# Optimization experiments

Hardware: AMD Instinct MI355X
Metric: run time of the kernel (lower is better)

The kernel has to match this reference:

```python
import jax, jax.numpy as jnp
import numpy as np

N = 50000        # nodes
E = 800000       # edges (avg degree 16)
MUL = 32         # multiplicity of 0e and 1o node-feature irreps
NA = 16          # node attr scalars (species embedding)
NB = 8           # edge radial basis size
FC_H = 64        # radial MLP hidden width
NPATH = 5        # tp paths: 0e*0e->0e, 0e*1o->1o, 1o*0e->1o, 1o*1o->0e, 1o*1o->1o
AVG_NEI = 16.0


def setup_inputs() -> dict:
    k = jax.random.split(jax.random.key(0), 16)
    return dict(
        node_feats=jax.random.normal(k[0], (N, 4 * MUL), jnp.float32),   # 32x0e + 32x1o
        node_attrs=jax.random.normal(k[1], (N, NA), jnp.float32),
        edge_embedding=jax.random.uniform(k[2], (E, NB), jnp.float32),
        edge_attrs=jax.random.normal(k[3], (E, 4), jnp.float32),         # SH l=0 (1) + l=1 (3)
        edge_src=jax.random.randint(k[4], (E,), 0, N),
        edge_dst=jax.random.randint(k[5], (E,), 0, N),
        W1_s=jax.random.normal(k[6], (MUL, MUL), jnp.float32) / np.sqrt(MUL),
        W1_v=jax.random.normal(k[7], (MUL, MUL), jnp.float32) / np.sqrt(MUL),
        fc_w1=jax.random.normal(k[8], (NB, FC_H), jnp.float32) / np.sqrt(NB),
        fc_b1=jnp.zeros((FC_H,), jnp.float32),
        fc_w2=jax.random.normal(k[9], (FC_H, NPATH * MUL), jnp.float32) / np.sqrt(FC_H),
        W2_s=jax.random.normal(k[10], (2 * MUL, 2 * MUL), jnp.float32) / np.sqrt(2 * MUL),
        W2_v=jax.random.normal(k[11], (3 * MUL, MUL), jnp.float32) / np.sqrt(3 * MUL),
        Wsc_s=jax.random.normal(k[12], (MUL, NA, 2 * MUL), jnp.float32) / np.sqrt(MUL * NA),
        Wsc_v=jax.random.normal(k[13], (MUL, NA, MUL), jnp.float32) / np.sqrt(MUL * NA),
    )


def reference(node_feats, node_attrs, edge_embedding, edge_attrs,
              edge_src, edge_dst, W1_s, W1_v, fc_w1, fc_b1, fc_w2,
              W2_s, W2_v, Wsc_s, Wsc_v):
    n = node_feats.shape[0]
    s = node_feats[:, :MUL]                        # [N, mul]     0e scalars
    v = node_feats[:, MUL:].reshape(n, MUL, 3)     # [N, mul, 3]  1o vectors

    # linear_1: per-irrep multiplicity mixing
    x_s = s @ W1_s
    x_v = jnp.einsum('nuc,uv->nvc', v, W1_v)

    # radial network -> per-edge tensor-product path weights (uvu, mul_in2 = 1)
    w = jax.nn.silu(edge_embedding @ fc_w1 + fc_b1) @ fc_w2   # [E, 5*mul]
    w00, w01, w10, w11s, w11v = [w[:, i * MUL:(i + 1) * MUL] for i in range(NPATH)]

    sh0 = edge_attrs[:, :1]     # [E, 1]  l=0
    sh1 = edge_attrs[:, 1:4]    # [E, 3]  l=1

    xs = x_s[edge_src]          # [E, mul]      gather source-node features
    xv = x_v[edge_src]          # [E, mul, 3]

    # Clebsch-Gordan tensor-product messages
    m_s0 = w00 * xs * sh0                                              # 0e x 0e -> 0e
    m_s1 = w11s * jnp.einsum('euc,ec->eu', xv, sh1) / np.sqrt(3.0)     # 1o x 1o -> 0e
    m_v0 = (w01 * xs)[:, :, None] * sh1[:, None, :]                    # 0e x 1o -> 1o
    m_v1 = w10[:, :, None] * xv * sh0[:, :, None]                      # 1o x 0e -> 1o
    m_v2 = w11v[:, :, None] * jnp.cross(
        xv, jnp.broadcast_to(sh1[:, None, :], xv.shape)) / np.sqrt(2.0)  # 1o x 1o -> 1o

    # scatter-sum to destination nodes, normalized by sqrt(avg num neighbors)
    inv = 1.0 / np.sqrt(AVG_NEI)
    a_s = jax.ops.segment_sum(jnp.concatenate([m_s0, m_s1], axis=1),
                              edge_dst, num_segments=n) * inv           # [N, 2*mul]
    a_v = jax.ops.segment_sum(jnp.concatenate([m_v0, m_v1, m_v2], axis=1),
                              edge_dst, num_segments=n) * inv           # [N, 3*mul, 3]

    # linear_2: mix tp paths into gated irreps (2*mul scalars + mul vectors)
    y_s = a_s @ W2_s
    y_v = jnp.einsum('nuc,uo->noc', a_v, W2_v)

    # self-connection: fully-connected tp of input feats with scalar node attrs
    y_s = y_s + jnp.einsum('nu,na,uao->no', s, node_attrs, Wsc_s)
    y_v = y_v + jnp.einsum('nuc,na,uao->noc', v, node_attrs, Wsc_v)

    # gate: first mul scalars -> silu output; next mul scalars -> silu gates on vectors
    out_s = jax.nn.silu(y_s[:, :MUL])
    gates = jax.nn.silu(y_s[:, MUL:])
    out_v = y_v * gates[:, :, None]

    out = jnp.concatenate([out_s, out_v.reshape(n, 3 * MUL)], axis=1)
    return node_feats + out   # resnet (irreps match)
```

## Files before the change

### kernel.cpp

```cpp
#include <hip/hip_runtime.h>

#define NN 50000
#define NE 800000

__device__ __forceinline__ float silu_f(float x) { return x / (1.0f + __expf(-x)); }

__global__ __launch_bounds__(256) void k_node_transform(
    const float* __restrict__ node_feats,
    const float* __restrict__ W1_s,
    const float* __restrict__ W1_v,
    float* __restrict__ xf)
{
    __shared__ float sW1s[32 * 32];
    __shared__ float sW1v[32 * 32];
    __shared__ float sfeat[8][128];
    int t = threadIdx.x;
    for (int i = t; i < 1024; i += 256) { sW1s[i] = W1_s[i]; sW1v[i] = W1_v[i]; }
    int nodeBase = blockIdx.x * 8;
    for (int i = t; i < 8 * 128; i += 256) {
        int nn = nodeBase + (i >> 7);
        sfeat[i >> 7][i & 127] = (nn < NN) ? node_feats[(long)nn * 128 + (i & 127)] : 0.0f;
    }
    __syncthreads();
    int g = t >> 5, o = t & 31;
    int n = nodeBase + g;
    if (n >= NN) return;
    float accs = 0.f, acc0 = 0.f, acc1 = 0.f, acc2 = 0.f;
#pragma unroll
    for (int u = 0; u < 32; ++u) {
        float su  = sfeat[g][u];
        float vu0 = sfeat[g][32 + u * 3 + 0];
        float vu1 = sfeat[g][32 + u * 3 + 1];
        float vu2 = sfeat[g][32 + u * 3 + 2];
        float ws = sW1s[u * 32 + o];
        float wv = sW1v[u * 32 + o];
        accs += su * ws;
        acc0 += vu0 * wv;
        acc1 += vu1 * wv;
        acc2 += vu2 * wv;
    }
    float4 r; r.x = accs; r.y = acc0; r.z = acc1; r.w = acc2;
    *(float4*)&xf[((long)n * 32 + o) * 4] = r;
}

__global__ __launch_bounds__(256) void k_hist(const int* __restrict__ edge_dst,
                                              int* __restrict__ counts)
{
    int e = blockIdx.x * 256 + threadIdx.x;
    if (e < NE) atomicAdd(&counts[edge_dst[e]], 1);
}

__global__ __launch_bounds__(1024) void k_scan(const int* __restrict__ counts,
                                               int* __restrict__ row_ptr,
                                               int* __restrict__ cursor)
{
    __shared__ int wsum[16];
    __shared__ int carry_s;
    int t = threadIdx.x;
    int lane = t & 63, w = t >> 6;
    if (t == 0) carry_s = 0;
    __syncthreads();
    for (int base = 0; base < NN; base += 1024) {
        int i = base + t;
        int v = (i < NN) ? counts[i] : 0;
        int s = v;
#pragma unroll
        for (int d = 1; d < 64; d <<= 1) {
            int o = __shfl_up(s, d, 64);
            if (lane >= d) s += o;
        }
        if (lane == 63) wsum[w] = s;
        __syncthreads();
        if (w == 0) {
            int ws = (lane < 16) ? wsum[lane] : 0;
#pragma unroll
            for (int d = 1; d < 16; d <<= 1) {
                int o = __shfl_up(ws, d, 64);
                if (lane >= d) ws += o;
            }
            if (lane < 16) wsum[lane] = ws;
        }
        __syncthreads();
        int excl = (s - v) + ((w > 0) ? wsum[w - 1] : 0) + carry_s;
        if (i < NN) { row_ptr[i] = excl; cursor[i] = excl; }
        int total = wsum[15];
        __syncthreads();
        if (t == 0) carry_s += total;
        __syncthreads();
    }
    if (t == 0) row_ptr[NN] = carry_s;
}

__global__ __launch_bounds__(256) void k_fill(const int* __restrict__ edge_dst,
                                              int* __restrict__ cursor,
                                              int* __restrict__ edge_ids)
{
    int e = blockIdx.x * 256 + threadIdx.x;
    if (e < NE) {
        int slot = atomicAdd(&cursor[edge_dst[e]], 1);
        edge_ids[slot] = e;
    }
}

__global__ __launch_bounds__(256, 3) void k_gather_t(
    const float* __restrict__ edge_embedding,
    const float* __restrict__ edge_attrs,
    const int*   __restrict__ edge_src,
    const float* __restrict__ fc_w1,
    const float* __restrict__ fc_b1,
    const float* __restrict__ fc_w2,
    const float* __restrict__ xf,
    const int*   __restrict__ row_ptr,
    const int*   __restrict__ edge_ids,
    const float* __restrict__ node_feats,
    const float* __restrict__ node_attrs,
    const float* __restrict__ W2_s,
    const float* __restrict__ W2_v,
    const float* __restrict__ Wsc_s,
    const float* __restrict__ Wsc_v,
    float* __restrict__ out)
{
    __shared__ __align__(16) float sw2t[160 * 68];
    __shared__ __align__(16) float hbuf[8][256];

    int t = threadIdx.x;
    for (int i = t; i < 64 * 160; i += 256) {
        int j = i / 160, c = i - j * 160;
        sw2t[c * 68 + j] = fc_w2[i];
    }
    __syncthreads();

    int g = t >> 5, lane = t & 31;
    int n = blockIdx.x * 8 + g;

    float w1a[8], w1b[8];
#pragma unroll
    for (int q = 0; q < 8; ++q) {
        w1a[q] = fc_w1[q * 64 + lane];
        w1b[q] = fc_w1[q * 64 + 32 + lane];
    }
    float b1a = fc_b1[lane], b1b = fc_b1[32 + lane];

    int start = row_ptr[n];
    int end   = row_ptr[n + 1];

    float as0 = 0.f, as1 = 0.f;
    float av[9];
#pragma unroll
    for (int p = 0; p < 9; ++p) av[p] = 0.f;

    float* hb = &hbuf[g][0];
    const float4* xf4 = (const float4*)xf;
    const float INV_SQRT3 = 0.5773502691896258f;
    const float INV_SQRT2 = 0.7071067811865476f;
    const float INV_NEI   = 0.25f;

    for (int i = start; i < end; i += 4) {
        int ne = end - i;
        int eid[4];
#pragma unroll
        for (int k = 0; k < 4; ++k) eid[k] = edge_ids[(k < ne) ? (i + k) : i];

        int srcv[4];
#pragma unroll
        for (int k = 0; k < 4; ++k) srcv[k] = edge_src[eid[k]];
        float4 at[4];
#pragma unroll
        for (int k = 0; k < 4; ++k) at[k] = *(const float4*)&edge_attrs[(long)eid[k] * 4];
        float4 xv[4];
#pragma unroll
        for (int k = 0; k < 4; ++k) xv[k] = xf4[(long)srcv[k] * 32 + lane];
        float em[4][8];
#pragma unroll
        for (int k = 0; k < 4; ++k) {
            *(float4*)&em[k][0] = *(const float4*)&edge_embedding[(long)eid[k] * 8];
            *(float4*)&em[k][4] = *(const float4*)&edge_embedding[(long)eid[k] * 8 + 4];
        }

#pragma unroll
        for (int k = 0; k < 4; ++k) {
            float h0 = b1a, h1 = b1b;
#pragma unroll
            for (int q = 0; q < 8; ++q) {
                float e = em[k][q];
                h0 += e * w1a[q];
                h1 += e * w1b[q];
            }
            hb[k * 64 + lane]      = silu_f(h0);
            hb[k * 64 + 32 + lane] = silu_f(h1);
        }

        float acc[5][4];
#pragma unroll
        for (int p = 0; p < 5; ++p)
#pragma unroll
            for (int k = 0; k < 4; ++k) acc[p][k] = 0.f;

#pragma unroll 2
        for (int jb = 0; jb < 16; ++jb) {
            float4 w0 = *(const float4*)&sw2t[(0 * 32 + lane) * 68 + jb * 4];
            float4 w1 = *(const float4*)&sw2t[(1 * 32 + lane) * 68 + jb * 4];
            float4 w2 = *(const float4*)&sw2t[(2 * 32 + lane) * 68 + jb * 4];
            float4 w3 = *(const float4*)&sw2t[(3 * 32 + lane) * 68 + jb * 4];
            float4 w4 = *(const float4*)&sw2t[(4 * 32 + lane) * 68 + jb * 4];
#pragma unroll
            for (int k = 0; k < 4; ++k) {
                float4 h4 = *(const float4*)&hb[k * 64 + jb * 4];
                acc[0][k] += h4.x * w0.x + h4.y * w0.y + h4.z * w0.z + h4.w * w0.w;
                acc[1][k] += h4.x * w1.x + h4.y * w1.y + h4.z * w1.z + h4.w * w1.w;
                acc[2][k] += h4.x * w2.x + h4.y * w2.y + h4.z * w2.z + h4.w * w2.w;
                acc[3][k] += h4.x * w3.x + h4.y * w3.y + h4.z * w3.z + h4.w * w3.w;
                acc[4][k] += h4.x * w4.x + h4.y * w4.y + h4.z * w4.z + h4.w * w4.w;
            }
        }

#pragma unroll
        for (int k = 0; k < 4; ++k) {
            if (k >= ne) break;
            float4 a4 = at[k];
            float xs  = xv[k].x;
            float xv0 = xv[k].y, xv1 = xv[k].z, xv2 = xv[k].w;
            float w00 = acc[0][k], w01 = acc[1][k], w10 = acc[2][k];
            float w11s = acc[3][k], w11v = acc[4][k];

            as0 += w00 * xs * a4.x;
            float dot = xv0 * a4.y + xv1 * a4.z + xv2 * a4.w;
            as1 += w11s * dot * INV_SQRT3;
            float t01 = w01 * xs;
            av[0] += t01 * a4.y; av[1] += t01 * a4.z; av[2] += t01 * a4.w;
            float t10 = w10 * a4.x;
            av[3] += t10 * xv0; av[4] += t10 * xv1; av[5] += t10 * xv2;
            float k2 = w11v * INV_SQRT2;
            av[6] += k2 * (xv1 * a4.w - xv2 * a4.z);
            av[7] += k2 * (xv2 * a4.y - xv0 * a4.w);
            av[8] += k2 * (xv0 * a4.z - xv1 * a4.y);
        }
    }

    __syncthreads();
    float* epi = sw2t + (g << 9);

    epi[lane]      = as0 * INV_NEI;
    epi[32 + lane] = as1 * INV_NEI;
#pragma unroll
    for (int p = 0; p < 3; ++p)
#pragma unroll
        for (int c = 0; c < 3; ++c)
            epi[64 + (p * 32 + lane) * 3 + c] = av[p * 3 + c] * INV_NEI;

    *(float4*)&hb[lane * 4] = *(const float4*)&node_feats[(long)n * 128 + lane * 4];
    if (lane < 16) hb[128 + lane] = node_attrs[(long)n * 16 + lane];

    int o = lane;
    float ys0 = 0.f, ys1 = 0.f, yv0 = 0.f, yv1 = 0.f, yv2 = 0.f;

#pragma unroll 8
    for (int u = 0; u < 64; ++u) {
        float as = epi[u];
        ys0 += as * W2_s[u * 64 + o];
        ys1 += as * W2_s[u * 64 + 32 + o];
    }
#pragma unroll 8
    for (int u = 0; u < 96; ++u) {
        float wv = W2_v[u * 32 + o];
        yv0 += epi[64 + u * 3 + 0] * wv;
        yv1 += epi[64 + u * 3 + 1] * wv;
        yv2 += epi[64 + u * 3 + 2] * wv;
    }

    float att[16];
#pragma unroll
    for (int a = 0; a < 16; ++a) att[a] = hb[128 + a];

    for (int u = 0; u < 32; ++u) {
        const float* Wsp = &Wsc_s[u * 1024 + o];
        const float* Wvp = &Wsc_v[u * 512 + o];
        float t0 = 0.f, t1 = 0.f, tv = 0.f;
#pragma unroll
        for (int a = 0; a < 16; ++a) {
            float aa = att[a];
            t0 += aa * Wsp[a * 64];
            t1 += aa * Wsp[a * 64 + 32];
            tv += aa * Wvp[a * 32];
        }
        float su = hb[u];
        ys0 += su * t0;
        ys1 += su * t1;
        float vv0 = hb[32 + u * 3 + 0];
        float vv1 = hb[32 + u * 3 + 1];
        float vv2 = hb[32 + u * 3 + 2];
        yv0 += vv0 * tv;
        yv1 += vv1 * tv;
        yv2 += vv2 * tv;
    }

    float os   = silu_f(ys0);
    float gate = silu_f(ys1);
    long base = (long)n * 128;
    out[base + o] = hb[o] + os;
    out[base + 32 + o * 3 + 0] = hb[32 + o * 3 + 0] + yv0 * gate;
    out[base + 32 + o * 3 + 1] = hb[32 + o * 3 + 1] + yv1 * gate;
    out[base + 32 + o * 3 + 2] = hb[32 + o * 3 + 2] + yv2 * gate;
}

extern "C" void kernel_launch(void* const* d_in, const int* in_sizes, int n_in,
                              void* d_out, int out_size, void* d_ws, size_t ws_size,
                              hipStream_t stream) {
    const float* node_feats     = (const float*)d_in[0];
    const float* node_attrs     = (const float*)d_in[1];
    const float* edge_embedding = (const float*)d_in[2];
    const float* edge_attrs     = (const float*)d_in[3];
    const int*   edge_src       = (const int*)d_in[4];
    const int*   edge_dst       = (const int*)d_in[5];
    const float* W1_s  = (const float*)d_in[6];
    const float* W1_v  = (const float*)d_in[7];
    const float* fc_w1 = (const float*)d_in[8];
    const float* fc_b1 = (const float*)d_in[9];
    const float* fc_w2 = (const float*)d_in[10];
    const float* W2_s  = (const float*)d_in[11];
    const float* W2_v  = (const float*)d_in[12];
    const float* Wsc_s = (const float*)d_in[13];
    const float* Wsc_v = (const float*)d_in[14];
    float* out = (float*)d_out;

    float* ws  = (float*)d_ws;
    float* xf  = ws;
    int* ibase    = (int*)(ws + (long)NN * 128);
    int* counts   = ibase;
    int* row_ptr  = ibase + NN;
    int* cursor   = ibase + 2 * NN + 1;
    int* edge_ids = ibase + 3 * NN + 1;

    hipMemsetAsync(counts, 0, (size_t)NN * sizeof(int), stream);
    k_hist<<<(NE + 255) / 256, 256, 0, stream>>>(edge_dst, counts);
    k_node_transform<<<(NN + 7) / 8, 256, 0, stream>>>(node_feats, W1_s, W1_v, xf);
    k_scan<<<1, 1024, 0, stream>>>(counts, row_ptr, cursor);
    k_fill<<<(NE + 255) / 256, 256, 0, stream>>>(edge_dst, cursor, edge_ids);
    k_gather_t<<<NN / 8, 256, 0, stream>>>(edge_embedding, edge_attrs, edge_src,
                                           fc_w1, fc_b1, fc_w2, xf,
                                           row_ptr, edge_ids,
                                           node_feats, node_attrs,
                                           W2_s, W2_v, Wsc_s, Wsc_v, out);
}
```

Measured before the change: 921.6 us.

## Use fp16 packed dot products for radial MLP second layer with 8-edge batches

The radial MLP hidden activations and the fc_w2 matrix are stored in shared memory as fp16 and combined with v_dot2 (fdot2) instructions that accumulate in fp32. This halves LDS traffic and instruction count for the dominant per-edge 64x160 matmul. Edges are now processed 8 at a time, the hidden-unit layout is interleaved in pairs, and the shared pool is shrunk and reused for the epilogue so occupancy can rise to 4 blocks per CU. The cost is reduced precision in the path weights and higher register pressure from the larger accumulator array.

```diff
diff --git a/kernel.cpp b/kernel.cpp
--- a/kernel.cpp
+++ b/kernel.cpp
@@ -3,7 +3,18 @@
 #define NN 50000
 #define NE 800000
 
+typedef _Float16 half2t __attribute__((ext_vector_type(2)));
+union H16 { float4 f; half2t p[4]; };
+
 __device__ __forceinline__ float silu_f(float x) { return x / (1.0f + __expf(-x)); }
+
+__device__ __forceinline__ float fdot2(half2t a, half2t b, float c) {
+#if __has_builtin(__builtin_amdgcn_fdot2)
+    return __builtin_amdgcn_fdot2(a, b, c, false);
+#else
+    return c + (float)a.x * (float)b.x + (float)a.y * (float)b.y;
+#endif
+}
 
 __global__ __launch_bounds__(256) void k_node_transform(
     const float* __restrict__ node_feats,
@@ -102,7 +113,10 @@
     }
 }
 
-__global__ __launch_bounds__(256, 3) void k_gather_t(
+#define SW2_HBYTES (160 * 72 * 2)
+#define POOL_BYTES (SW2_HBYTES + 8 * 8 * 128)
+
+__global__ __launch_bounds__(256, 4) void k_gather_t(
     const float* __restrict__ edge_embedding,
     const float* __restrict__ edge_attrs,
     const int*   __restrict__ edge_src,
@@ -120,13 +134,14 @@
     const float* __restrict__ Wsc_v,
     float* __restrict__ out)
 {
-    __shared__ __align__(16) float sw2t[160 * 68];
-    __shared__ __align__(16) float hbuf[8][256];
+    __shared__ __align__(16) unsigned char pool[POOL_BYTES];
+    _Float16* swp = (_Float16*)pool;
+    half2t*   hhp = (half2t*)(pool + SW2_HBYTES);
 
     int t = threadIdx.x;
     for (int i = t; i < 64 * 160; i += 256) {
         int j = i / 160, c = i - j * 160;
-        sw2t[c * 68 + j] = fc_w2[i];
+        swp[c * 72 + j] = (_Float16)fc_w2[i];
     }
     __syncthreads();
 
@@ -136,10 +151,10 @@
     float w1a[8], w1b[8];
 #pragma unroll
     for (int q = 0; q < 8; ++q) {
-        w1a[q] = fc_w1[q * 64 + lane];
-        w1b[q] = fc_w1[q * 64 + 32 + lane];
-    }
-    float b1a = fc_b1[lane], b1b = fc_b1[32 + lane];
+        w1a[q] = fc_w1[q * 64 + 2 * lane];
+        w1b[q] = fc_w1[q * 64 + 2 * lane + 1];
+    }
+    float b1a = fc_b1[2 * lane], b1b = fc_b1[2 * lane + 1];
 
     int start = row_ptr[n];
     int end   = row_ptr[n + 1];
@@ -149,96 +164,101 @@
 #pragma unroll
     for (int p = 0; p < 9; ++p) av[p] = 0.f;
 
-    float* hb = &hbuf[g][0];
     const float4* xf4 = (const float4*)xf;
+    half2t* hme = hhp + g * (8 * 32);
     const float INV_SQRT3 = 0.5773502691896258f;
     const float INV_SQRT2 = 0.7071067811865476f;
     const float INV_NEI   = 0.25f;
 
-    for (int i = start; i < end; i += 4) {
-        int ne = end - i;
-        int eid[4];
-#pragma unroll
-        for (int k = 0; k < 4; ++k) eid[k] = edge_ids[(k < ne) ? (i + k) : i];
-
-        int srcv[4];
-#pragma unroll
-        for (int k = 0; k < 4; ++k) srcv[k] = edge_src[eid[k]];
-        float4 at[4];
-#pragma unroll
-        for (int k = 0; k < 4; ++k) at[k] = *(const float4*)&edge_attrs[(long)eid[k] * 4];
-        float4 xv[4];
-#pragma unroll
-        for (int k = 0; k < 4; ++k) xv[k] = xf4[(long)srcv[k] * 32 + lane];
-        float em[4][8];
-#pragma unroll
-        for (int k = 0; k < 4; ++k) {
-            *(float4*)&em[k][0] = *(const float4*)&edge_embedding[(long)eid[k] * 8];
-            *(float4*)&em[k][4] = *(const float4*)&edge_embedding[(long)eid[k] * 8 + 4];
-        }
-
-#pragma unroll
-        for (int k = 0; k < 4; ++k) {
+    for (int i0 = start; i0 < end; i0 += 8) {
+        int ne = end - i0;
+        int eid[8];
+#pragma unroll
+        for (int k = 0; k < 8; ++k) eid[k] = edge_ids[(k < ne) ? (i0 + k) : i0];
+
+#pragma unroll
+        for (int k = 0; k < 8; ++k) {
+            float4 e0 = *(const float4*)&edge_embedding[(long)eid[k] * 8];
+            float4 e1 = *(const float4*)&edge_embedding[(long)eid[k] * 8 + 4];
             float h0 = b1a, h1 = b1b;
-#pragma unroll
-            for (int q = 0; q < 8; ++q) {
-                float e = em[k][q];
-                h0 += e * w1a[q];
-                h1 += e * w1b[q];
+            h0 += e0.x * w1a[0] + e0.y * w1a[1] + e0.z * w1a[2] + e0.w * w1a[3];
+            h0 += e1.x * w1a[4] + e1.y * w1a[5] + e1.z * w1a[6] + e1.w * w1a[7];
+            h1 += e0.x * w1b[0] + e0.y * w1b[1] + e0.z * w1b[2] + e0.w * w1b[3];
+            h1 += e1.x * w1b[4] + e1.y * w1b[5] + e1.z * w1b[6] + e1.w * w1b[7];
+            half2t hp;
+            hp.x = (_Float16)silu_f(h0);
+            hp.y = (_Float16)silu_f(h1);
+            hme[k * 32 + lane] = hp;
+        }
+
+        float acc[5][8];
+#pragma unroll
+        for (int p = 0; p < 5; ++p)
+#pragma unroll
+            for (int k = 0; k < 8; ++k) acc[p][k] = 0.f;
+
+#pragma unroll 2
+        for (int jq = 0; jq < 8; ++jq) {
+            H16 w0, w1, w2, w3, w4;
+            w0.f = *(const float4*)&swp[(0 * 32 + lane) * 72 + jq * 8];
+            w1.f = *(const float4*)&swp[(1 * 32 + lane) * 72 + jq * 8];
+            w2.f = *(const float4*)&swp[(2 * 32 + lane) * 72 + jq * 8];
+            w3.f = *(const float4*)&swp[(3 * 32 + lane) * 72 + jq * 8];
+            w4.f = *(const float4*)&swp[(4 * 32 + lane) * 72 + jq * 8];
+#pragma unroll
+            for (int k = 0; k < 8; ++k) {
+                H16 hv;
+                hv.f = *(const float4*)&hme[k * 32 + jq * 4];
+#pragma unroll
+                for (int m = 0; m < 4; ++m) {
+                    acc[0][k] = fdot2(hv.p[m], w0.p[m], acc[0][k]);
+                    acc[1][k] = fdot2(hv.p[m], w1.p[m], acc[1][k]);
+                    acc[2][k] = fdot2(hv.p[m], w2.p[m], acc[2][k]);
+                    acc[3][k] = fdot2(hv.p[m], w3.p[m], acc[3][k]);
+                    acc[4][k] = fdot2(hv.p[m], w4.p[m], acc[4][k]);
+                }
             }
-            hb[k * 64 + lane]      = silu_f(h0);
-            hb[k * 64 + 32 + lane] = silu_f(h1);
-        }
-
-        float acc[5][4];
-#pragma unroll
-        for (int p = 0; p < 5; ++p)
-#pragma unroll
-            for (int k = 0; k < 4; ++k) acc[p][k] = 0.f;
-
-#pragma unroll 2
-        for (int jb = 0; jb < 16; ++jb) {
-            float4 w0 = *(const float4*)&sw2t[(0 * 32 + lane) * 68 + jb * 4];
-            float4 w1 = *(const float4*)&sw2t[(1 * 32 + lane) * 68 + jb * 4];
-            float4 w2 = *(const float4*)&sw2t[(2 * 32 + lane) * 68 + jb * 4];
-            float4 w3 = *(const float4*)&sw2t[(3 * 32 + lane) * 68 + jb * 4];
-            float4 w4 = *(const float4*)&sw2t[(4 * 32 + lane) * 68 + jb * 4];
+        }
+
+#pragma unroll
+        for (int h0i = 0; h0i < 8; h0i += 4) {
+            if (h0i >= ne) break;
+            int srcv[4];
+#pragma unroll
+            for (int k = 0; k < 4; ++k) srcv[k] = edge_src[eid[h0i + k]];
+            float4 at[4], xv[4];
 #pragma unroll
             for (int k = 0; k < 4; ++k) {
-                float4 h4 = *(const float4*)&hb[k * 64 + jb * 4];
-                acc[0][k] += h4.x * w0.x + h4.y * w0.y + h4.z * w0.z + h4.w * w0.w;
-                acc[1][k] += h4.x * w1.x + h4.y * w1.y + h4.z * w1.z + h4.w * w1.w;
-                acc[2][k] += h4.x * w2.x + h4.y * w2.y + h4.z * w2.z + h4.w * w2.w;
-                acc[3][k] += h4.x * w3.x + h4.y * w3.y + h4.z * w3.z + h4.w * w3.w;
-                acc[4][k] += h4.x * w4.x + h4.y * w4.y + h4.z * w4.z + h4.w * w4.w;
+                at[k] = *(const float4*)&edge_attrs[(long)eid[h0i + k] * 4];
+                xv[k] = xf4[(long)srcv[k] * 32 + lane];
             }
-        }
-
-#pragma unroll
-        for (int k = 0; k < 4; ++k) {
-            if (k >= ne) break;
-            float4 a4 = at[k];
-            float xs  = xv[k].x;
-            float xv0 = xv[k].y, xv1 = xv[k].z, xv2 = xv[k].w;
-            float w00 = acc[0][k], w01 = acc[1][k], w10 = acc[2][k];
-            float w11s = acc[3][k], w11v = acc[4][k];
-
-            as0 += w00 * xs * a4.x;
-            float dot = xv0 * a4.y + xv1 * a4.z + xv2 * a4.w;
-            as1 += w11s * dot * INV_SQRT3;
-            float t01 = w01 * xs;
-            av[0] += t01 * a4.y; av[1] += t01 * a4.z; av[2] += t01 * a4.w;
-            float t10 = w10 * a4.x;
-            av[3] += t10 * xv0; av[4] += t10 * xv1; av[5] += t10 * xv2;
-            float k2 = w11v * INV_SQRT2;
-            av[6] += k2 * (xv1 * a4.w - xv2 * a4.z);
-            av[7] += k2 * (xv2 * a4.y - xv0 * a4.w);
-            av[8] += k2 * (xv0 * a4.z - xv1 * a4.y);
+#pragma unroll
+            for (int k = 0; k < 4; ++k) {
+                int kk = h0i + k;
+                if (kk >= ne) break;
+                float4 a4 = at[k];
+                float xs  = xv[k].x;
+                float xv0 = xv[k].y, xv1 = xv[k].z, xv2 = xv[k].w;
+                float w00 = acc[0][kk], w01 = acc[1][kk], w10 = acc[2][kk];
+                float w11s = acc[3][kk], w11v = acc[4][kk];
+
+                as0 += w00 * xs * a4.x;
+                float dot = xv0 * a4.y + xv1 * a4.z + xv2 * a4.w;
+                as1 += w11s * dot * INV_SQRT3;
+                float t01 = w01 * xs;
+                av[0] += t01 * a4.y; av[1] += t01 * a4.z; av[2] += t01 * a4.w;
+                float t10 = w10 * a4.x;
+                av[3] += t10 * xv0; av[4] += t10 * xv1; av[5] += t10 * xv2;
+                float k2 = w11v * INV_SQRT2;
+                av[6] += k2 * (xv1 * a4.w - xv2 * a4.z);
+                av[7] += k2 * (xv2 * a4.y - xv0 * a4.w);
+                av[8] += k2 * (xv0 * a4.z - xv1 * a4.y);
+            }
         }
     }
 
     __syncthreads();
-    float* epi = sw2t + (g << 9);
+    float* epi = (float*)pool + (g << 9);
 
     epi[lane]      = as0 * INV_NEI;
     epi[32 + lane] = as1 * INV_NEI;
@@ -248,8 +268,8 @@
         for (int c = 0; c < 3; ++c)
             epi[64 + (p * 32 + lane) * 3 + c] = av[p * 3 + c] * INV_NEI;
 
-    *(float4*)&hb[lane * 4] = *(const float4*)&node_feats[(long)n * 128 + lane * 4];
-    if (lane < 16) hb[128 + lane] = node_attrs[(long)n * 16 + lane];
+    *(float4*)&epi[352 + lane * 4] = *(const float4*)&node_feats[(long)n * 128 + lane * 4];
+    if (lane < 16) epi[480 + lane] = node_attrs[(long)n * 16 + lane];
 
     int o = lane;
     float ys0 = 0.f, ys1 = 0.f, yv0 = 0.f, yv1 = 0.f, yv2 = 0.f;
@@ -270,7 +290,7 @@
 
     float att[16];
 #pragma unroll
-    for (int a = 0; a < 16; ++a) att[a] = hb[128 + a];
+    for (int a = 0; a < 16; ++a) att[a] = epi[480 + a];
 
     for (int u = 0; u < 32; ++u) {
         const float* Wsp = &Wsc_s[u * 1024 + o];
@@ -283,24 +303,21 @@
             t1 += aa * Wsp[a * 64 + 32];
             tv += aa * Wvp[a * 32];
         }
-        float su = hb[u];
+        float su = epi[352 + u];
         ys0 += su * t0;
         ys1 += su * t1;
-        float vv0 = hb[32 + u * 3 + 0];
-        float vv1 = hb[32 + u * 3 + 1];
-        float vv2 = hb[32 + u * 3 + 2];
-        yv0 += vv0 * tv;
-        yv1 += vv1 * tv;
-        yv2 += vv2 * tv;
+        yv0 += epi[352 + 32 + u * 3 + 0] * tv;
+        yv1 += epi[352 + 32 + u * 3 + 1] * tv;
+        yv2 += epi[352 + 32 + u * 3 + 2] * tv;
     }
 
     float os   = silu_f(ys0);
     float gate = silu_f(ys1);
     long base = (long)n * 128;
-    out[base + o] = hb[o] + os;
-    out[base + 32 + o * 3 + 0] = hb[32 + o * 3 + 0] + yv0 * gate;
-    out[base + 32 + o * 3 + 1] = hb[32 + o * 3 + 1] + yv1 * gate;
-    out[base + 32 + o * 3 + 2] = hb[32 + o * 3 + 2] + yv2 * gate;
+    out[base + o] = epi[352 + o] + os;
+    out[base + 32 + o * 3 + 0] = epi[352 + 32 + o * 3 + 0] + yv0 * gate;
+    out[base + 32 + o * 3 + 1] = epi[352 + 32 + o * 3 + 1] + yv1 * gate;
+    out[base + 32 + o * 3 + 2] = epi[352 + 32 + o * 3 + 2] + yv2 * gate;
 }
 
 extern "C" void kernel_launch(void* const* d_in, const int* in_sizes, int n_in,
```

Result: faster. 807.3 us (-12.4%).
